# Kernel optimization log

Hardware: AMD Instinct MI355X
Metric: run time of the kernel (lower is better)

Reference implementation:

```python
import jax, jax.numpy as jnp
import numpy as np

MAT_MODE = [(0, 1), (0, 2), (1, 2)]   # plane axes per component (TensoRF VM)
VEC_MODE = [2, 1, 0]                  # line axis per component
DISTANCE_SCALE = 1.0
WHITE_BG = True


def _bilinear(plane, uv):
    """plane: [C,H,W]; uv: [P,2] in [-1,1] (uv[:,0]->W, uv[:,1]->H). align_corners=True."""
    H, W = plane.shape[-2], plane.shape[-1]
    x = (uv[:, 0] + 1.0) * 0.5 * (W - 1)
    y = (uv[:, 1] + 1.0) * 0.5 * (H - 1)
    x0 = jnp.clip(jnp.floor(x), 0, W - 2).astype(jnp.int32)
    y0 = jnp.clip(jnp.floor(y), 0, H - 2).astype(jnp.int32)
    wx = x - x0
    wy = y - y0
    v00 = plane[:, y0, x0]
    v01 = plane[:, y0, x0 + 1]
    v10 = plane[:, y0 + 1, x0]
    v11 = plane[:, y0 + 1, x0 + 1]
    top = v00 * (1 - wx) + v01 * wx
    bot = v10 * (1 - wx) + v11 * wx
    return top * (1 - wy) + bot * wy   # [C,P]


def _linear1d(line, t):
    """line: [C,L]; t: [P] in [-1,1]. align_corners=True."""
    L = line.shape[-1]
    x = (t + 1.0) * 0.5 * (L - 1)
    x0 = jnp.clip(jnp.floor(x), 0, L - 2).astype(jnp.int32)
    w = x - x0
    return line[:, x0] * (1 - w) + line[:, x0 + 1] * w   # [C,P]


def setup_inputs() -> dict:
    key = jax.random.key(0)
    ks = jax.random.split(key, 8)
    N_rays = 4096
    # camera origins on a sphere of radius 4, dirs aimed at points inside the box
    o = jax.random.normal(ks[0], (N_rays, 3), jnp.float32)
    o = o / jnp.linalg.norm(o, axis=-1, keepdims=True) * 4.0
    tgt = jax.random.uniform(ks[1], (N_rays, 3), jnp.float32, -0.5, 0.5)
    d = tgt - o
    d = d / jnp.linalg.norm(d, axis=-1, keepdims=True)
    rays = jnp.concatenate([o, d], axis=-1)
    return {
        "rays": rays,
        "density_plane": 0.1 * jax.random.normal(ks[2], (3, 16, 256, 256), jnp.float32),
        "density_line": 0.1 * jax.random.normal(ks[3], (3, 16, 256), jnp.float32),
        "app_plane": 0.1 * jax.random.normal(ks[4], (3, 24, 256, 256), jnp.float32),
        "app_line": 0.1 * jax.random.normal(ks[5], (3, 24, 256), jnp.float32),
        "basis_mat": 0.1 * jax.random.normal(ks[6], (72, 3), jnp.float32),
        "aabb": jnp.array([[-1.5, -1.5, -1.5], [1.5, 1.5, 1.5]], jnp.float32),
        "N_samples": 256,
    }


def reference(rays, density_plane, density_line, app_plane, app_line, basis_mat, aabb, N_samples):
    N = rays.shape[0]
    o, d = rays[:, :3], rays[:, 3:6]
    # ray / aabb intersection
    vec = jnp.where(jnp.abs(d) < 1e-6, 1e-6, d)
    rate_a = (aabb[1] - o) / vec
    rate_b = (aabb[0] - o) / vec
    t_min = jnp.clip(jnp.minimum(rate_a, rate_b).max(-1), 0.05)
    t_max = jnp.maximum(jnp.maximum(rate_a, rate_b).min(-1), t_min + 1e-3)
    s = jnp.linspace(0.0, 1.0, N_samples, dtype=jnp.float32)
    z = t_min[:, None] * (1.0 - s) + t_max[:, None] * s          # [N,S]
    dists = jnp.diff(z, axis=-1)
    dists = jnp.concatenate([dists, dists[:, -1:]], axis=-1)      # [N,S]
    pts = o[:, None, :] + d[:, None, :] * z[..., None]            # [N,S,3]
    coords = (pts - aabb[0]) / (aabb[1] - aabb[0]) * 2.0 - 1.0
    inside = jnp.all(jnp.abs(coords) <= 1.0, axis=-1)             # [N,S]
    cf = coords.reshape(-1, 3)                                    # [P,3]

    sigma_feat = 0.0
    app_feats = []
    for i in range(3):
        uv = cf[:, list(MAT_MODE[i])]
        w = cf[:, VEC_MODE[i]]
        sigma_feat = sigma_feat + (_bilinear(density_plane[i], uv) * _linear1d(density_line[i], w)).sum(0)
        app_feats.append(_bilinear(app_plane[i], uv) * _linear1d(app_line[i], w))
    app = jnp.concatenate(app_feats, axis=0).T                    # [P, 72]

    sigma = jax.nn.softplus(sigma_feat).reshape(N, -1) * inside   # [N,S]
    alpha = 1.0 - jnp.exp(-sigma * dists * DISTANCE_SCALE)        # [N,S]
    T = jnp.cumprod(1.0 - alpha + 1e-10, axis=-1)
    T = jnp.concatenate([jnp.ones_like(T[:, :1]), T[:, :-1]], axis=-1)
    weights = alpha * T                                           # [N,S]

    rgb = jax.nn.sigmoid(app @ basis_mat).reshape(N, -1, 3)       # [N,S,3]
    rgb_map = (weights[..., None] * rgb).sum(1)                   # [N,3]
    acc = weights.sum(-1)
    if WHITE_BG:
        rgb_map = rgb_map + (1.0 - acc)[..., None]
    rgb_map = jnp.clip(rgb_map, 0.0, 1.0)
    depth_map = (weights * z).sum(-1, keepdims=True)              # [N,1]
    return rgb_map, depth_map
```

## Files before the change

kernel.cpp:

```cpp
#include <hip/hip_runtime.h>
#include <hip/hip_fp16.h>
#include <cmath>

#define NRAYS 4096
#define NSAMP 256

static constexpr size_t DPT_B = 0;
static constexpr size_t DLT_B = 3145728;
static constexpr size_t APT_B = DLT_B + 24576;
static constexpr size_t ALT_B = APT_B + 6291456;
static constexpr size_t RAY_B = ALT_B + 24576;
static constexpr size_t WS_NEED = RAY_B + 131072;

typedef _Float16 __attribute__((ext_vector_type(2))) v2h;
typedef __attribute__((ext_vector_type(2))) float f32x2;

#if defined(__has_builtin)
#if __has_builtin(__builtin_amdgcn_cvt_scalef32_pk_f16_fp8)
#define HAS_SCVT 1
#endif
#endif
#ifndef HAS_SCVT
#define HAS_SCVT 0
#endif

__device__ __forceinline__ float dot2acc(__half2 a, __half2 b, float c) {
  return __builtin_amdgcn_fdot2(__builtin_bit_cast(v2h, a),
                                __builtin_bit_cast(v2h, b), c, false);
}

__device__ __forceinline__ __half2 lerp2(__half2 a, __half2 b, __half2 w) {
  return __hfma2(w, __hsub2(b, a), a);
}

__device__ __forceinline__ void ld8h(const __half* p, __half2 h[4]) {
  uint4 r = *(const uint4*)p;
  h[0] = __builtin_bit_cast(__half2, r.x);
  h[1] = __builtin_bit_cast(__half2, r.y);
  h[2] = __builtin_bit_cast(__half2, r.z);
  h[3] = __builtin_bit_cast(__half2, r.w);
}

__device__ __forceinline__ unsigned pack2h(float a, float b) {
  return __builtin_bit_cast(unsigned, __floats2half2_rn(a, b));
}

__device__ __forceinline__ void dec4f8h(unsigned w, __half2& h0, __half2& h1) {
#if HAS_SCVT
  v2h a = __builtin_amdgcn_cvt_scalef32_pk_f16_fp8((int)w, 1.0f, false);
  v2h b = __builtin_amdgcn_cvt_scalef32_pk_f16_fp8((int)w, 1.0f, true);
  h0 = __builtin_bit_cast(__half2, a);
  h1 = __builtin_bit_cast(__half2, b);
#else
  f32x2 lo = __builtin_amdgcn_cvt_pk_f32_fp8((int)w, false);
  f32x2 hi = __builtin_amdgcn_cvt_pk_f32_fp8((int)w, true);
  h0 = __floats2half2_rn(lo.x, lo.y);
  h1 = __floats2half2_rn(hi.x, hi.y);
#endif
}

__device__ __forceinline__ void dec8f8(uint2 q, __half2 h[4]) {
  dec4f8h(q.x, h[0], h[1]);
  dec4f8h(q.y, h[2], h[3]);
}

__device__ __forceinline__ void dec16f8(uint4 q, __half2 h[8]) {
  dec4f8h(q.x, h[0], h[1]);
  dec4f8h(q.y, h[2], h[3]);
  dec4f8h(q.z, h[4], h[5]);
  dec4f8h(q.w, h[6], h[7]);
}

__device__ __forceinline__ unsigned pk4f8(float a, float b, float c, float d) {
  int w = __builtin_amdgcn_cvt_pk_fp8_f32(a, b, 0, false);
  w = __builtin_amdgcn_cvt_pk_fp8_f32(c, d, w, true);
  return (unsigned)w;
}

__device__ __forceinline__ void grid_uv(float c, int& i0, float& w) {
  float f = (c + 1.0f) * 127.5f;
  float fl = floorf(f);
  fl = fminf(fmaxf(fl, 0.0f), 254.0f);
  i0 = (int)fl;
  w = f - fl;
}

__device__ __forceinline__ void bilin_w(float wx, float wy, __half2& W00,
                                        __half2& W01, __half2& W10, __half2& W11) {
  float ix = 1.0f - wx, iy = 1.0f - wy;
  W00 = __float2half2_rn(ix * iy);
  W01 = __float2half2_rn(wx * iy);
  W10 = __float2half2_rn(ix * wy);
  W11 = __float2half2_rn(wx * wy);
}

__global__ __launch_bounds__(256) void prep_kernel(
    const float* __restrict__ dp, const float* __restrict__ ap,
    const float* __restrict__ dl, const float* __restrict__ al,
    const float* __restrict__ rays, const float* __restrict__ aabb,
    unsigned char* __restrict__ dpt, unsigned char* __restrict__ apt,
    __half* __restrict__ dlt, unsigned char* __restrict__ alt,
    float4* __restrict__ rd) {
  int b = blockIdx.x, x = threadIdx.x;
  if (b < 768) {
    int i = b >> 8, y = b & 255;
    const float* src = dp + (size_t)(i * 16) * 65536 + y * 256 + x;
    float f[16];
#pragma unroll
    for (int c = 0; c < 16; ++c) f[c] = src[c * 65536];
    uint4 v;
    v.x = pk4f8(f[0], f[1], f[2], f[3]);
    v.y = pk4f8(f[4], f[5], f[6], f[7]);
    v.z = pk4f8(f[8], f[9], f[10], f[11]);
    v.w = pk4f8(f[12], f[13], f[14], f[15]);
    *(uint4*)(dpt + ((size_t)(i << 16) + (y << 8) + x) * 16) = v;
  } else if (b < 1536) {
    int t = b - 768;
    int i = t >> 8, y = t & 255;
    const float* src = ap + (size_t)(i * 24) * 65536 + y * 256 + x;
    float f[24];
#pragma unroll
    for (int c = 0; c < 24; ++c) f[c] = src[c * 65536];
    uint4 v0, v1;
    v0.x = pk4f8(f[0], f[1], f[2], f[3]);
    v0.y = pk4f8(f[4], f[5], f[6], f[7]);
    v0.z = pk4f8(f[8], f[9], f[10], f[11]);
    v0.w = pk4f8(f[12], f[13], f[14], f[15]);
    v1.x = pk4f8(f[16], f[17], f[18], f[19]);
    v1.y = pk4f8(f[20], f[21], f[22], f[23]);
    v1.z = 0u; v1.w = 0u;
    uint4* dst = (uint4*)(apt + ((size_t)(i << 16) + (y << 8) + x) * 32);
    dst[0] = v0; dst[1] = v1;
  } else if (b < 1539) {
    int i = b - 1536, l = x;
    float f[16];
#pragma unroll
    for (int c = 0; c < 16; ++c) f[c] = dl[(i * 16 + c) * 256 + l];
    uint4 v0, v1;
    v0.x = pack2h(f[0], f[1]);   v0.y = pack2h(f[2], f[3]);
    v0.z = pack2h(f[4], f[5]);   v0.w = pack2h(f[6], f[7]);
    v1.x = pack2h(f[8], f[9]);   v1.y = pack2h(f[10], f[11]);
    v1.z = pack2h(f[12], f[13]); v1.w = pack2h(f[14], f[15]);
    uint4* dst = (uint4*)(dlt + (i * 256 + l) * 16);
    dst[0] = v0; dst[1] = v1;
  } else if (b < 1542) {
    int i = b - 1539, l = x;
    float f[24];
#pragma unroll
    for (int c = 0; c < 24; ++c) f[c] = al[(i * 24 + c) * 256 + l];
    uint4 v0, v1;
    v0.x = pk4f8(f[0], f[1], f[2], f[3]);
    v0.y = pk4f8(f[4], f[5], f[6], f[7]);
    v0.z = pk4f8(f[8], f[9], f[10], f[11]);
    v0.w = pk4f8(f[12], f[13], f[14], f[15]);
    v1.x = pk4f8(f[16], f[17], f[18], f[19]);
    v1.y = pk4f8(f[20], f[21], f[22], f[23]);
    v1.z = 0u; v1.w = 0u;
    uint4* dst = (uint4*)(alt + (i * 256 + l) * 32);
    dst[0] = v0; dst[1] = v1;
  } else {
    int r = (b - 1542) * 256 + x;
    if (r < NRAYS) {
      float o0 = rays[r * 6 + 0], o1 = rays[r * 6 + 1], o2 = rays[r * 6 + 2];
      float d0 = rays[r * 6 + 3], d1 = rays[r * 6 + 4], d2 = rays[r * 6 + 5];
      float A0 = aabb[0], A1 = aabb[1], A2 = aabb[2];
      float B0 = aabb[3], B1 = aabb[4], B2 = aabb[5];
      float v0 = fabsf(d0) < 1e-6f ? 1e-6f : d0;
      float v1 = fabsf(d1) < 1e-6f ? 1e-6f : d1;
      float v2 = fabsf(d2) < 1e-6f ? 1e-6f : d2;
      float ra0 = (B0 - o0) / v0, rb0 = (A0 - o0) / v0;
      float ra1 = (B1 - o1) / v1, rb1 = (A1 - o1) / v1;
      float ra2 = (B2 - o2) / v2, rb2 = (A2 - o2) / v2;
      float tmin = fmaxf(fmaxf(fminf(ra0, rb0), fminf(ra1, rb1)), fminf(ra2, rb2));
      tmin = fmaxf(tmin, 0.05f);
      float tmax = fminf(fminf(fmaxf(ra0, rb0), fmaxf(ra1, rb1)), fmaxf(ra2, rb2));
      tmax = fmaxf(tmax, tmin + 0.001f);
      float dt = (tmax - tmin) * (1.0f / 255.0f);
      float s0 = 2.0f / (B0 - A0), s1 = 2.0f / (B1 - A1), s2 = 2.0f / (B2 - A2);
      float4 a2, b2;
      a2.x = (o0 - A0) * s0 - 1.0f; a2.y = (o1 - A1) * s1 - 1.0f;
      a2.z = (o2 - A2) * s2 - 1.0f; a2.w = tmin;
      b2.x = d0 * s0; b2.y = d1 * s1; b2.z = d2 * s2; b2.w = dt;
      rd[r * 2] = a2;
      rd[r * 2 + 1] = b2;
    }
  }
}

__device__ __forceinline__ float density_f8(const unsigned char* __restrict__ pl,
                                            const __half* __restrict__ ln,
                                            int x0, int y0, int l0,
                                            __half2 W00, __half2 W01,
                                            __half2 W10, __half2 W11,
                                            __half2 wl, int sub, float acc) {
  const unsigned char* p = pl + (size_t)((y0 * 256 + x0) << 4) + sub * 8;
  uint2 q00 = *(const uint2*)p;
  uint2 q01 = *(const uint2*)(p + 16);
  uint2 q10 = *(const uint2*)(p + 4096);
  uint2 q11 = *(const uint2*)(p + 4096 + 16);
  __half2 A[4], B[4], C[4], D[4], la[4], lb[4];
  dec8f8(q00, A); dec8f8(q01, B); dec8f8(q10, C); dec8f8(q11, D);
  const __half* lp = ln + (l0 << 4) + sub * 8;
  ld8h(lp, la); ld8h(lp + 16, lb);
#pragma unroll
  for (int r = 0; r < 4; ++r) {
    __half2 m = __hmul2(W00, A[r]);
    m = __hfma2(W01, B[r], m);
    m = __hfma2(W10, C[r], m);
    m = __hfma2(W11, D[r], m);
    __half2 l = lerp2(la[r], lb[r], wl);
    acc = dot2acc(m, l, acc);
  }
  return acc;
}

__device__ __forceinline__ void app_f8(const unsigned char* __restrict__ pl,
                                       const unsigned char* __restrict__ ln,
                                       const __half2* __restrict__ btR,
                                       const __half2* __restrict__ btG,
                                       const __half2* __restrict__ btB,
                                       int x0, int y0, int l0,
                                       __half2 W00, __half2 W01,
                                       __half2 W10, __half2 W11,
                                       __half2 wl, int sub,
                                       float& dr, float& dg, float& db) {
  const unsigned char* p = pl + ((size_t)(y0 * 256 + x0) << 5) + sub * 16;
  uint4 qA = *(const uint4*)p;
  uint4 qB = *(const uint4*)(p + 32);
  uint4 qC = *(const uint4*)(p + 8192);
  uint4 qD = *(const uint4*)(p + 8192 + 32);
  const unsigned char* lp = ln + (l0 << 5) + sub * 16;
  uint4 qLA = *(const uint4*)lp;
  uint4 qLB = *(const uint4*)(lp + 32);
  __half2 A[8], B[8], C[8], D[8], LA[8], LB[8];
  dec16f8(qA, A); dec16f8(qB, B); dec16f8(qC, C); dec16f8(qD, D);
  dec16f8(qLA, LA); dec16f8(qLB, LB);
#pragma unroll
  for (int r = 0; r < 8; ++r) {
    __half2 m = __hmul2(W00, A[r]);
    m = __hfma2(W01, B[r], m);
    m = __hfma2(W10, C[r], m);
    m = __hfma2(W11, D[r], m);
    __half2 l = lerp2(LA[r], LB[r], wl);
    __half2 av = __hmul2(m, l);
    dr = dot2acc(av, btR[r], dr);
    dg = dot2acc(av, btG[r], dg);
    db = dot2acc(av, btB[r], db);
  }
}

__global__ __launch_bounds__(512) void render_fused(
    const float4* __restrict__ rd, const float* __restrict__ basis,
    const unsigned char* __restrict__ dpt, const __half* __restrict__ dlt,
    const unsigned char* __restrict__ apt, const unsigned char* __restrict__ alt,
    float* __restrict__ out) {
  __shared__ __align__(16) __half bth[3][3][32];
  __shared__ __align__(16) float4 sm[NSAMP];
  int tid = threadIdx.x;
  if (tid < 288) {
    int k = tid / 96, rem = tid - k * 96;
    int m = rem >> 5, c = rem & 31;
    float v = (c < 24) ? basis[(m * 24 + c) * 3 + k] : 0.0f;
    bth[k][m][c] = __float2half(v);
  }

  int ray = blockIdx.x;
  int j = tid >> 1, sub = tid & 1;

  float4 ra = rd[ray * 2];
  float4 rb = rd[ray * 2 + 1];
  float z = fmaf((float)j, rb.w, ra.w);
  float c0 = fmaf(rb.x, z, ra.x);
  float c1 = fmaf(rb.y, z, ra.y);
  float c2 = fmaf(rb.z, z, ra.z);
  bool inside = (fabsf(c0) <= 1.0f) && (fabsf(c1) <= 1.0f) && (fabsf(c2) <= 1.0f);

  __syncthreads();

  float sig = 0.f, dr = 0.f, dg = 0.f, db = 0.f;
  if (inside) {
    int i0, i1, i2;
    float w0, w1, w2;
    grid_uv(c0, i0, w0);
    grid_uv(c1, i1, w1);
    grid_uv(c2, i2, w2);
    __half2 h0 = __float2half2_rn(w0);
    __half2 h1 = __float2half2_rn(w1);
    __half2 h2 = __float2half2_rn(w2);
    __half2 Wa00, Wa01, Wa10, Wa11;
    __half2 Wb00, Wb01, Wb10, Wb11;
    __half2 Wc00, Wc01, Wc10, Wc11;
    bilin_w(w0, w1, Wa00, Wa01, Wa10, Wa11);
    bilin_w(w0, w2, Wb00, Wb01, Wb10, Wb11);
    bilin_w(w1, w2, Wc00, Wc01, Wc10, Wc11);

    sig = density_f8(dpt + 0 * 1048576, dlt + 0 * 4096, i0, i1, i2,
                     Wa00, Wa01, Wa10, Wa11, h2, sub, sig);
    sig = density_f8(dpt + 1 * 1048576, dlt + 1 * 4096, i0, i2, i1,
                     Wb00, Wb01, Wb10, Wb11, h1, sub, sig);
    sig = density_f8(dpt + 2 * 1048576, dlt + 2 * 4096, i1, i2, i0,
                     Wc00, Wc01, Wc10, Wc11, h0, sub, sig);
    app_f8(apt + 0 * 2097152, alt + 0 * 8192,
           (const __half2*)&bth[0][0][sub * 16], (const __half2*)&bth[1][0][sub * 16],
           (const __half2*)&bth[2][0][sub * 16], i0, i1, i2,
           Wa00, Wa01, Wa10, Wa11, h2, sub, dr, dg, db);
    app_f8(apt + 1 * 2097152, alt + 1 * 8192,
           (const __half2*)&bth[0][1][sub * 16], (const __half2*)&bth[1][1][sub * 16],
           (const __half2*)&bth[2][1][sub * 16], i0, i2, i1,
           Wb00, Wb01, Wb10, Wb11, h1, sub, dr, dg, db);
    app_f8(apt + 2 * 2097152, alt + 2 * 8192,
           (const __half2*)&bth[0][2][sub * 16], (const __half2*)&bth[1][2][sub * 16],
           (const __half2*)&bth[2][2][sub * 16], i1, i2, i0,
           Wc00, Wc01, Wc10, Wc11, h0, sub, dr, dg, db);
  }
  sig += __shfl_xor(sig, 1, 64);
  dr += __shfl_xor(dr, 1, 64);
  dg += __shfl_xor(dg, 1, 64);
  db += __shfl_xor(db, 1, 64);

  if (sub == 0) {
    float e = __expf(-fabsf(sig));
    float sp = fmaxf(sig, 0.f) + __logf(1.0f + e);
    float4 sv;
    sv.x = inside ? (1.0f - __expf(-sp * rb.w)) : 0.0f;
    sv.y = __builtin_amdgcn_rcpf(1.0f + __expf(-dr));
    sv.z = __builtin_amdgcn_rcpf(1.0f + __expf(-dg));
    sv.w = __builtin_amdgcn_rcpf(1.0f + __expf(-db));
    sm[j] = sv;
  }
  __syncthreads();

  if (tid < 64) {
    int lane = tid;
    float tmin = ra.w, dt = rb.w;
    float C = 1.0f;
    float racc = 0.f, gacc = 0.f, bacc = 0.f, wsum = 0.f, dsum = 0.f;
    for (int q = 0; q < 4; ++q) {
      int jj = q * 64 + lane;
      float4 sv = sm[jj];
      float alpha = sv.x;
      float zz = fmaf((float)jj, dt, tmin);
      float p = 1.0f - alpha + 1e-10f;
#pragma unroll
      for (int off = 1; off < 64; off <<= 1) {
        float t = __shfl_up(p, off, 64);
        if (lane >= off) p *= t;
      }
      float tot = __shfl(p, 63, 64);
      float e = __shfl_up(p, 1, 64);
      if (lane == 0) e = 1.0f;
      float Tj = C * e;
      float w = alpha * Tj;
      racc += w * sv.y;
      gacc += w * sv.z;
      bacc += w * sv.w;
      wsum += w;
      dsum += w * zz;
      C *= tot;
    }
#pragma unroll
    for (int off = 32; off > 0; off >>= 1) {
      racc += __shfl_down(racc, off, 64);
      gacc += __shfl_down(gacc, off, 64);
      bacc += __shfl_down(bacc, off, 64);
      wsum += __shfl_down(wsum, off, 64);
      dsum += __shfl_down(dsum, off, 64);
    }
    if (lane == 0) {
      float bgw = 1.0f - wsum;
      out[ray * 3 + 0] = fminf(fmaxf(racc + bgw, 0.f), 1.f);
      out[ray * 3 + 1] = fminf(fmaxf(gacc + bgw, 0.f), 1.f);
      out[ray * 3 + 2] = fminf(fmaxf(bacc + bgw, 0.f), 1.f);
      out[NRAYS * 3 + ray] = dsum;
    }
  }
}

__device__ __forceinline__ float density_orig(const float* __restrict__ plane,
                                              const float* __restrict__ line,
                                              float cx, float cy, float cw) {
  int x0, y0, l0; float wx, wy, wl;
  grid_uv(cx, x0, wx); grid_uv(cy, y0, wy); grid_uv(cw, l0, wl);
  int base = y0 * 256 + x0;
  float s = 0.0f;
#pragma unroll 4
  for (int c = 0; c < 16; ++c) {
    const float* pc = plane + c * 65536;
    float v00 = pc[base], v01 = pc[base + 1];
    float v10 = pc[base + 256], v11 = pc[base + 257];
    float top = fmaf(wx, v01 - v00, v00);
    float bot = fmaf(wx, v11 - v10, v10);
    float mid = fmaf(wy, bot - top, top);
    float la = line[c * 256 + l0], lb = line[c * 256 + l0 + 1];
    float lv = fmaf(wl, lb - la, la);
    s += mid * lv;
  }
  return s;
}

__device__ __forceinline__ void app_orig(const float* __restrict__ plane,
                                         const float* __restrict__ line,
                                         const float* __restrict__ btR,
                                         const float* __restrict__ btG,
                                         const float* __restrict__ btB,
                                         float cx, float cy, float cw,
                                         float& dr, float& dg, float& db) {
  int x0, y0, l0; float wx, wy, wl;
  grid_uv(cx, x0, wx); grid_uv(cy, y0, wy); grid_uv(cw, l0, wl);
  int base = y0 * 256 + x0;
#pragma unroll 4
  for (int c = 0; c < 24; ++c) {
    const float* pc = plane + c * 65536;
    float v00 = pc[base], v01 = pc[base + 1];
    float v10 = pc[base + 256], v11 = pc[base + 257];
    float top = fmaf(wx, v01 - v00, v00);
    float bot = fmaf(wx, v11 - v10, v10);
    float mid = fmaf(wy, bot - top, top);
    float la = line[c * 256 + l0], lb = line[c * 256 + l0 + 1];
    float lv = fmaf(wl, lb - la, la);
    float av = mid * lv;
    dr += av * btR[c]; dg += av * btG[c]; db += av * btB[c];
  }
}

__global__ __launch_bounds__(256) void render_fallback(
    const float* __restrict__ rays, const float* __restrict__ basis,
    const float* __restrict__ aabb, const float* __restrict__ dplane,
    const float* __restrict__ dline, const float* __restrict__ aplane,
    const float* __restrict__ aline, float* __restrict__ out) {
  __shared__ float bt[3 * 72];
  int tid = threadIdx.x;
  if (tid < 216) {
    int k = tid / 72, r = tid - k * 72;
    bt[tid] = basis[r * 3 + k];
  }
  __syncthreads();
  int lane = tid & 63;
  int ray = blockIdx.x * 4 + (tid >> 6);

  float o0 = rays[ray * 6 + 0], o1 = rays[ray * 6 + 1], o2 = rays[ray * 6 + 2];
  float d0 = rays[ray * 6 + 3], d1 = rays[ray * 6 + 4], d2 = rays[ray * 6 + 5];
  float A0 = aabb[0], A1 = aabb[1], A2 = aabb[2];
  float B0 = aabb[3], B1 = aabb[4], B2 = aabb[5];
  float v0 = fabsf(d0) < 1e-6f ? 1e-6f : d0;
  float v1 = fabsf(d1) < 1e-6f ? 1e-6f : d1;
  float v2 = fabsf(d2) < 1e-6f ? 1e-6f : d2;
  float ra0 = (B0 - o0) / v0, rb0 = (A0 - o0) / v0;
  float ra1 = (B1 - o1) / v1, rb1 = (A1 - o1) / v1;
  float ra2 = (B2 - o2) / v2, rb2 = (A2 - o2) / v2;
  float tmin = fmaxf(fmaxf(fminf(ra0, rb0), fminf(ra1, rb1)), fminf(ra2, rb2));
  tmin = fmaxf(tmin, 0.05f);
  float tmax = fminf(fminf(fmaxf(ra0, rb0), fmaxf(ra1, rb1)), fmaxf(ra2, rb2));
  tmax = fmaxf(tmax, tmin + 0.001f);
  float dt = (tmax - tmin) * (1.0f / 255.0f);
  float s0 = 2.0f / (B0 - A0), s1 = 2.0f / (B1 - A1), s2 = 2.0f / (B2 - A2);

  float C = 1.0f;
  float racc = 0.f, gacc = 0.f, bacc = 0.f, wsum = 0.f, dsum = 0.f;
  for (int q = 0; q < 4; ++q) {
    int j = q * 64 + lane;
    float sfrac = (float)j * (1.0f / 255.0f);
    float z = tmin * (1.0f - sfrac) + tmax * sfrac;
    float c0 = (o0 + d0 * z - A0) * s0 - 1.0f;
    float c1 = (o1 + d1 * z - A1) * s1 - 1.0f;
    float c2 = (o2 + d2 * z - A2) * s2 - 1.0f;
    bool inside = (fabsf(c0) <= 1.0f) && (fabsf(c1) <= 1.0f) && (fabsf(c2) <= 1.0f);
    float alpha = 0.f, cr = 0.f, cg = 0.f, cb = 0.f;
    if (inside) {
      float sig = 0.f, dr = 0.f, dg = 0.f, db = 0.f;
      sig += density_orig(dplane + 0 * 1048576, dline + 0 * 4096, c0, c1, c2);
      sig += density_orig(dplane + 1 * 1048576, dline + 1 * 4096, c0, c2, c1);
      sig += density_orig(dplane + 2 * 1048576, dline + 2 * 4096, c1, c2, c0);
      app_orig(aplane + 0 * 1572864, aline + 0 * 6144,
               &bt[0 * 72 + 0], &bt[1 * 72 + 0], &bt[2 * 72 + 0],
               c0, c1, c2, dr, dg, db);
      app_orig(aplane + 1 * 1572864, aline + 1 * 6144,
               &bt[0 * 72 + 24], &bt[1 * 72 + 24], &bt[2 * 72 + 24],
               c0, c2, c1, dr, dg, db);
      app_orig(aplane + 2 * 1572864, aline + 2 * 6144,
               &bt[0 * 72 + 48], &bt[1 * 72 + 48], &bt[2 * 72 + 48],
               c1, c2, c0, dr, dg, db);
      float sp = fmaxf(sig, 0.f) + log1pf(expf(-fabsf(sig)));
      alpha = 1.0f - expf(-sp * dt);
      cr = 1.0f / (1.0f + expf(-dr));
      cg = 1.0f / (1.0f + expf(-dg));
      cb = 1.0f / (1.0f + expf(-db));
    }
    float p = 1.0f - alpha + 1e-10f;
#pragma unroll
    for (int off = 1; off < 64; off <<= 1) {
      float t = __shfl_up(p, off, 64);
      if (lane >= off) p *= t;
    }
    float tot = __shfl(p, 63, 64);
    float e = __shfl_up(p, 1, 64);
    if (lane == 0) e = 1.0f;
    float Tj = C * e;
    float w = alpha * Tj;
    racc += w * cr; gacc += w * cg; bacc += w * cb;
    wsum += w; dsum += w * z;
    C *= tot;
  }
#pragma unroll
  for (int off = 32; off > 0; off >>= 1) {
    racc += __shfl_down(racc, off, 64);
    gacc += __shfl_down(gacc, off, 64);
    bacc += __shfl_down(bacc, off, 64);
    wsum += __shfl_down(wsum, off, 64);
    dsum += __shfl_down(dsum, off, 64);
  }
  if (lane == 0) {
    float bgw = 1.0f - wsum;
    out[ray * 3 + 0] = fminf(fmaxf(racc + bgw, 0.f), 1.f);
    out[ray * 3 + 1] = fminf(fmaxf(gacc + bgw, 0.f), 1.f);
    out[ray * 3 + 2] = fminf(fmaxf(bacc + bgw, 0.f), 1.f);
    out[NRAYS * 3 + ray] = dsum;
  }
}

extern "C" void kernel_launch(void* const* d_in, const int* in_sizes, int n_in,
                              void* d_out, int out_size, void* d_ws, size_t ws_size,
                              hipStream_t stream) {
  const float* rays  = (const float*)d_in[0];
  const float* dp    = (const float*)d_in[1];
  const float* dl    = (const float*)d_in[2];
  const float* ap    = (const float*)d_in[3];
  const float* al    = (const float*)d_in[4];
  const float* basis = (const float*)d_in[5];
  const float* aabb  = (const float*)d_in[6];
  float* out = (float*)d_out;

  if (ws_size >= WS_NEED) {
    char* ws = (char*)d_ws;
    unsigned char* dpt = (unsigned char*)(ws + DPT_B);
    __half* dlt = (__half*)(ws + DLT_B);
    unsigned char* apt = (unsigned char*)(ws + APT_B);
    unsigned char* alt = (unsigned char*)(ws + ALT_B);
    float4* rayd = (float4*)(ws + RAY_B);
    prep_kernel<<<1558, 256, 0, stream>>>(dp, ap, dl, al, rays, aabb,
                                          dpt, apt, dlt, alt, rayd);
    render_fused<<<NRAYS, 512, 0, stream>>>(rayd, basis, dpt, dlt, apt, alt, out);
  } else {
    render_fallback<<<NRAYS / 4, 256, 0, stream>>>(
        rays, basis, aabb, dp, dl, ap, al, out);
  }
}
```

Measured before the change: 154.8 us.

## Split padded 32-byte FP8 appearance texels into 16+8 byte planes

Appearance plane and line features were stored as 32 bytes per texel in FP8, with 8 bytes of zero padding. They are now split into a 16-byte array for channels 0-15 and an 8-byte array for channels 16-23. Each of the two sub-lanes reads 8+4 bytes per corner instead of 16, and the basis table in shared memory is permuted to match the new channel order. This removes the padding from gather traffic and shrinks the appearance texture footprint, which may improve cache hit rates. The cost is twice as many separate, smaller load instructions per corner.

```diff
diff --git a/kernel.cpp b/kernel.cpp
--- a/kernel.cpp
+++ b/kernel.cpp
@@ -5,11 +5,13 @@
 #define NRAYS 4096
 #define NSAMP 256
 
-static constexpr size_t DPT_B = 0;
-static constexpr size_t DLT_B = 3145728;
-static constexpr size_t APT_B = DLT_B + 24576;
-static constexpr size_t ALT_B = APT_B + 6291456;
-static constexpr size_t RAY_B = ALT_B + 24576;
+static constexpr size_t DPT_B  = 0;
+static constexpr size_t DLT_B  = 3145728;
+static constexpr size_t APTA_B = DLT_B + 24576;
+static constexpr size_t APTB_B = APTA_B + 3145728;
+static constexpr size_t ALTA_B = APTB_B + 1572864;
+static constexpr size_t ALTB_B = ALTA_B + 12288;
+static constexpr size_t RAY_B  = ALTB_B + 6144;
 static constexpr size_t WS_NEED = RAY_B + 131072;
 
 typedef _Float16 __attribute__((ext_vector_type(2))) v2h;
@@ -64,13 +66,6 @@
   dec4f8h(q.y, h[2], h[3]);
 }
 
-__device__ __forceinline__ void dec16f8(uint4 q, __half2 h[8]) {
-  dec4f8h(q.x, h[0], h[1]);
-  dec4f8h(q.y, h[2], h[3]);
-  dec4f8h(q.z, h[4], h[5]);
-  dec4f8h(q.w, h[6], h[7]);
-}
-
 __device__ __forceinline__ unsigned pk4f8(float a, float b, float c, float d) {
   int w = __builtin_amdgcn_cvt_pk_fp8_f32(a, b, 0, false);
   w = __builtin_amdgcn_cvt_pk_fp8_f32(c, d, w, true);
@@ -98,8 +93,9 @@
     const float* __restrict__ dp, const float* __restrict__ ap,
     const float* __restrict__ dl, const float* __restrict__ al,
     const float* __restrict__ rays, const float* __restrict__ aabb,
-    unsigned char* __restrict__ dpt, unsigned char* __restrict__ apt,
-    __half* __restrict__ dlt, unsigned char* __restrict__ alt,
+    unsigned char* __restrict__ dpt, unsigned char* __restrict__ aptA,
+    unsigned char* __restrict__ aptB, __half* __restrict__ dlt,
+    unsigned char* __restrict__ altA, unsigned char* __restrict__ altB,
     float4* __restrict__ rd) {
   int b = blockIdx.x, x = threadIdx.x;
   if (b < 768) {
@@ -121,16 +117,17 @@
     float f[24];
 #pragma unroll
     for (int c = 0; c < 24; ++c) f[c] = src[c * 65536];
-    uint4 v0, v1;
-    v0.x = pk4f8(f[0], f[1], f[2], f[3]);
-    v0.y = pk4f8(f[4], f[5], f[6], f[7]);
-    v0.z = pk4f8(f[8], f[9], f[10], f[11]);
-    v0.w = pk4f8(f[12], f[13], f[14], f[15]);
-    v1.x = pk4f8(f[16], f[17], f[18], f[19]);
-    v1.y = pk4f8(f[20], f[21], f[22], f[23]);
-    v1.z = 0u; v1.w = 0u;
-    uint4* dst = (uint4*)(apt + ((size_t)(i << 16) + (y << 8) + x) * 32);
-    dst[0] = v0; dst[1] = v1;
+    uint4 vA;
+    vA.x = pk4f8(f[0], f[1], f[2], f[3]);
+    vA.y = pk4f8(f[4], f[5], f[6], f[7]);
+    vA.z = pk4f8(f[8], f[9], f[10], f[11]);
+    vA.w = pk4f8(f[12], f[13], f[14], f[15]);
+    uint2 vB;
+    vB.x = pk4f8(f[16], f[17], f[18], f[19]);
+    vB.y = pk4f8(f[20], f[21], f[22], f[23]);
+    size_t idx = (size_t)(i << 16) + (y << 8) + x;
+    *(uint4*)(aptA + idx * 16) = vA;
+    *(uint2*)(aptB + idx * 8) = vB;
   } else if (b < 1539) {
     int i = b - 1536, l = x;
     float f[16];
@@ -148,16 +145,16 @@
     float f[24];
 #pragma unroll
     for (int c = 0; c < 24; ++c) f[c] = al[(i * 24 + c) * 256 + l];
-    uint4 v0, v1;
-    v0.x = pk4f8(f[0], f[1], f[2], f[3]);
-    v0.y = pk4f8(f[4], f[5], f[6], f[7]);
-    v0.z = pk4f8(f[8], f[9], f[10], f[11]);
-    v0.w = pk4f8(f[12], f[13], f[14], f[15]);
-    v1.x = pk4f8(f[16], f[17], f[18], f[19]);
-    v1.y = pk4f8(f[20], f[21], f[22], f[23]);
-    v1.z = 0u; v1.w = 0u;
-    uint4* dst = (uint4*)(alt + (i * 256 + l) * 32);
-    dst[0] = v0; dst[1] = v1;
+    uint4 vA;
+    vA.x = pk4f8(f[0], f[1], f[2], f[3]);
+    vA.y = pk4f8(f[4], f[5], f[6], f[7]);
+    vA.z = pk4f8(f[8], f[9], f[10], f[11]);
+    vA.w = pk4f8(f[12], f[13], f[14], f[15]);
+    uint2 vB;
+    vB.x = pk4f8(f[16], f[17], f[18], f[19]);
+    vB.y = pk4f8(f[20], f[21], f[22], f[23]);
+    *(uint4*)(altA + (i * 256 + l) * 16) = vA;
+    *(uint2*)(altB + (i * 256 + l) * 8) = vB;
   } else {
     int r = (b - 1542) * 256 + x;
     if (r < NRAYS) {
@@ -214,29 +211,45 @@
   return acc;
 }
 
-__device__ __forceinline__ void app_f8(const unsigned char* __restrict__ pl,
-                                       const unsigned char* __restrict__ ln,
-                                       const __half2* __restrict__ btR,
-                                       const __half2* __restrict__ btG,
-                                       const __half2* __restrict__ btB,
-                                       int x0, int y0, int l0,
-                                       __half2 W00, __half2 W01,
-                                       __half2 W10, __half2 W11,
-                                       __half2 wl, int sub,
-                                       float& dr, float& dg, float& db) {
-  const unsigned char* p = pl + ((size_t)(y0 * 256 + x0) << 5) + sub * 16;
-  uint4 qA = *(const uint4*)p;
-  uint4 qB = *(const uint4*)(p + 32);
-  uint4 qC = *(const uint4*)(p + 8192);
-  uint4 qD = *(const uint4*)(p + 8192 + 32);
-  const unsigned char* lp = ln + (l0 << 5) + sub * 16;
-  uint4 qLA = *(const uint4*)lp;
-  uint4 qLB = *(const uint4*)(lp + 32);
-  __half2 A[8], B[8], C[8], D[8], LA[8], LB[8];
-  dec16f8(qA, A); dec16f8(qB, B); dec16f8(qC, C); dec16f8(qD, D);
-  dec16f8(qLA, LA); dec16f8(qLB, LB);
-#pragma unroll
-  for (int r = 0; r < 8; ++r) {
+__device__ __forceinline__ void app_f8s(const unsigned char* __restrict__ plA,
+                                        const unsigned char* __restrict__ plB,
+                                        const unsigned char* __restrict__ lnA,
+                                        const unsigned char* __restrict__ lnB,
+                                        const __half2* __restrict__ btR,
+                                        const __half2* __restrict__ btG,
+                                        const __half2* __restrict__ btB,
+                                        int x0, int y0, int l0,
+                                        __half2 W00, __half2 W01,
+                                        __half2 W10, __half2 W11,
+                                        __half2 wl, int sub,
+                                        float& dr, float& dg, float& db) {
+  size_t base = (size_t)(y0 * 256 + x0);
+  const unsigned char* pA = plA + (base << 4) + sub * 8;
+  uint2 a00 = *(const uint2*)pA;
+  uint2 a01 = *(const uint2*)(pA + 16);
+  uint2 a10 = *(const uint2*)(pA + 4096);
+  uint2 a11 = *(const uint2*)(pA + 4096 + 16);
+  const unsigned char* pB = plB + (base << 3) + sub * 4;
+  unsigned b00 = *(const unsigned*)pB;
+  unsigned b01 = *(const unsigned*)(pB + 8);
+  unsigned b10 = *(const unsigned*)(pB + 2048);
+  unsigned b11 = *(const unsigned*)(pB + 2048 + 8);
+  const unsigned char* lA = lnA + (l0 << 4) + sub * 8;
+  uint2 la2 = *(const uint2*)lA;
+  uint2 lb2 = *(const uint2*)(lA + 16);
+  const unsigned char* lB = lnB + (l0 << 3) + sub * 4;
+  unsigned la1 = *(const unsigned*)lB;
+  unsigned lb1 = *(const unsigned*)(lB + 8);
+
+  __half2 A[6], B[6], C[6], D[6], LA[6], LB[6];
+  dec8f8(a00, A); dec4f8h(b00, A[4], A[5]);
+  dec8f8(a01, B); dec4f8h(b01, B[4], B[5]);
+  dec8f8(a10, C); dec4f8h(b10, C[4], C[5]);
+  dec8f8(a11, D); dec4f8h(b11, D[4], D[5]);
+  dec8f8(la2, LA); dec4f8h(la1, LA[4], LA[5]);
+  dec8f8(lb2, LB); dec4f8h(lb1, LB[4], LB[5]);
+#pragma unroll
+  for (int r = 0; r < 6; ++r) {
     __half2 m = __hmul2(W00, A[r]);
     m = __hfma2(W01, B[r], m);
     m = __hfma2(W10, C[r], m);
@@ -252,16 +265,18 @@
 __global__ __launch_bounds__(512) void render_fused(
     const float4* __restrict__ rd, const float* __restrict__ basis,
     const unsigned char* __restrict__ dpt, const __half* __restrict__ dlt,
-    const unsigned char* __restrict__ apt, const unsigned char* __restrict__ alt,
+    const unsigned char* __restrict__ aptA, const unsigned char* __restrict__ aptB,
+    const unsigned char* __restrict__ altA, const unsigned char* __restrict__ altB,
     float* __restrict__ out) {
-  __shared__ __align__(16) __half bth[3][3][32];
+  __shared__ __align__(16) __half bthp[3][3][24];
   __shared__ __align__(16) float4 sm[NSAMP];
   int tid = threadIdx.x;
-  if (tid < 288) {
-    int k = tid / 96, rem = tid - k * 96;
-    int m = rem >> 5, c = rem & 31;
-    float v = (c < 24) ? basis[(m * 24 + c) * 3 + k] : 0.0f;
-    bth[k][m][c] = __float2half(v);
+  if (tid < 216) {
+    int k = tid / 72, rem = tid - k * 72;
+    int m = rem / 24, t = rem - m * 24;
+    int s = t / 12, u = t - s * 12;
+    int ch = (u < 8) ? (s * 8 + u) : (16 + s * 4 + (u - 8));
+    bthp[k][m][t] = __float2half(basis[(m * 24 + ch) * 3 + k]);
   }
 
   int ray = blockIdx.x;
@@ -300,18 +315,19 @@
                      Wb00, Wb01, Wb10, Wb11, h1, sub, sig);
     sig = density_f8(dpt + 2 * 1048576, dlt + 2 * 4096, i1, i2, i0,
                      Wc00, Wc01, Wc10, Wc11, h0, sub, sig);
-    app_f8(apt + 0 * 2097152, alt + 0 * 8192,
-           (const __half2*)&bth[0][0][sub * 16], (const __half2*)&bth[1][0][sub * 16],
-           (const __half2*)&bth[2][0][sub * 16], i0, i1, i2,
-           Wa00, Wa01, Wa10, Wa11, h2, sub, dr, dg, db);
-    app_f8(apt + 1 * 2097152, alt + 1 * 8192,
-           (const __half2*)&bth[0][1][sub * 16], (const __half2*)&bth[1][1][sub * 16],
-           (const __half2*)&bth[2][1][sub * 16], i0, i2, i1,
-           Wb00, Wb01, Wb10, Wb11, h1, sub, dr, dg, db);
-    app_f8(apt + 2 * 2097152, alt + 2 * 8192,
-           (const __half2*)&bth[0][2][sub * 16], (const __half2*)&bth[1][2][sub * 16],
-           (const __half2*)&bth[2][2][sub * 16], i1, i2, i0,
-           Wc00, Wc01, Wc10, Wc11, h0, sub, dr, dg, db);
+    int bo = sub * 12;
+    app_f8s(aptA + 0 * 1048576, aptB + 0 * 524288, altA + 0 * 4096, altB + 0 * 2048,
+            (const __half2*)&bthp[0][0][bo], (const __half2*)&bthp[1][0][bo],
+            (const __half2*)&bthp[2][0][bo], i0, i1, i2,
+            Wa00, Wa01, Wa10, Wa11, h2, sub, dr, dg, db);
+    app_f8s(aptA + 1 * 1048576, aptB + 1 * 524288, altA + 1 * 4096, altB + 1 * 2048,
+            (const __half2*)&bthp[0][1][bo], (const __half2*)&bthp[1][1][bo],
+            (const __half2*)&bthp[2][1][bo], i0, i2, i1,
+            Wb00, Wb01, Wb10, Wb11, h1, sub, dr, dg, db);
+    app_f8s(aptA + 2 * 1048576, aptB + 2 * 524288, altA + 2 * 4096, altB + 2 * 2048,
+            (const __half2*)&bthp[0][2][bo], (const __half2*)&bthp[1][2][bo],
+            (const __half2*)&bthp[2][2][bo], i1, i2, i0,
+            Wc00, Wc01, Wc10, Wc11, h0, sub, dr, dg, db);
   }
   sig += __shfl_xor(sig, 1, 64);
   dr += __shfl_xor(dr, 1, 64);
@@ -532,14 +548,17 @@
 
   if (ws_size >= WS_NEED) {
     char* ws = (char*)d_ws;
-    unsigned char* dpt = (unsigned char*)(ws + DPT_B);
-    __half* dlt = (__half*)(ws + DLT_B);
-    unsigned char* apt = (unsigned char*)(ws + APT_B);
-    unsigned char* alt = (unsigned char*)(ws + ALT_B);
-    float4* rayd = (float4*)(ws + RAY_B);
+    unsigned char* dpt  = (unsigned char*)(ws + DPT_B);
+    __half* dlt         = (__half*)(ws + DLT_B);
+    unsigned char* aptA = (unsigned char*)(ws + APTA_B);
+    unsigned char* aptB = (unsigned char*)(ws + APTB_B);
+    unsigned char* altA = (unsigned char*)(ws + ALTA_B);
+    unsigned char* altB = (unsigned char*)(ws + ALTB_B);
+    float4* rayd        = (float4*)(ws + RAY_B);
     prep_kernel<<<1558, 256, 0, stream>>>(dp, ap, dl, al, rays, aabb,
-                                          dpt, apt, dlt, alt, rayd);
-    render_fused<<<NRAYS, 512, 0, stream>>>(rayd, basis, dpt, dlt, apt, alt, out);
+                                          dpt, aptA, aptB, dlt, altA, altB, rayd);
+    render_fused<<<NRAYS, 512, 0, stream>>>(rayd, basis, dpt, dlt,
+                                            aptA, aptB, altA, altB, out);
   } else {
     render_fallback<<<NRAYS / 4, 256, 0, stream>>>(
         rays, basis, aabb, dp, dl, ap, al, out);
```

New measurement: 169.6 us. +9.6%, slower.

## Process one sample per thread instead of splitting channels across thread pairs

Applied to the files above, without the earlier changes.

Each thread now handles all channels of a sample, so blocks drop from 512 to 256 threads and the shuffle reduction between thread pairs goes away. Appearance channels are read as 24 packed bytes (uint4 plus uint2) with no padding to 32, and the basis table in shared memory shrinks to match. This halves thread count and skips the padded channels, but each thread now holds more registers and has more memory latency to hide per lane.

```diff
diff --git a/kernel.cpp b/kernel.cpp
--- a/kernel.cpp
+++ b/kernel.cpp
@@ -57,18 +57,6 @@
   h0 = __floats2half2_rn(lo.x, lo.y);
   h1 = __floats2half2_rn(hi.x, hi.y);
 #endif
-}
-
-__device__ __forceinline__ void dec8f8(uint2 q, __half2 h[4]) {
-  dec4f8h(q.x, h[0], h[1]);
-  dec4f8h(q.y, h[2], h[3]);
-}
-
-__device__ __forceinline__ void dec16f8(uint4 q, __half2 h[8]) {
-  dec4f8h(q.x, h[0], h[1]);
-  dec4f8h(q.y, h[2], h[3]);
-  dec4f8h(q.z, h[4], h[5]);
-  dec4f8h(q.w, h[6], h[7]);
 }
 
 __device__ __forceinline__ unsigned pk4f8(float a, float b, float c, float d) {
@@ -187,85 +175,115 @@
   }
 }
 
-__device__ __forceinline__ float density_f8(const unsigned char* __restrict__ pl,
-                                            const __half* __restrict__ ln,
-                                            int x0, int y0, int l0,
-                                            __half2 W00, __half2 W01,
-                                            __half2 W10, __half2 W11,
-                                            __half2 wl, int sub, float acc) {
-  const unsigned char* p = pl + (size_t)((y0 * 256 + x0) << 4) + sub * 8;
-  uint2 q00 = *(const uint2*)p;
-  uint2 q01 = *(const uint2*)(p + 16);
-  uint2 q10 = *(const uint2*)(p + 4096);
-  uint2 q11 = *(const uint2*)(p + 4096 + 16);
-  __half2 A[4], B[4], C[4], D[4], la[4], lb[4];
-  dec8f8(q00, A); dec8f8(q01, B); dec8f8(q10, C); dec8f8(q11, D);
-  const __half* lp = ln + (l0 << 4) + sub * 8;
-  ld8h(lp, la); ld8h(lp + 16, lb);
-#pragma unroll
-  for (int r = 0; r < 4; ++r) {
-    __half2 m = __hmul2(W00, A[r]);
-    m = __hfma2(W01, B[r], m);
-    m = __hfma2(W10, C[r], m);
-    m = __hfma2(W11, D[r], m);
-    __half2 l = lerp2(la[r], lb[r], wl);
-    acc = dot2acc(m, l, acc);
+__device__ __forceinline__ float density_full(const unsigned char* __restrict__ pl,
+                                              const __half* __restrict__ ln,
+                                              int x0, int y0, int l0,
+                                              __half2 W00, __half2 W01,
+                                              __half2 W10, __half2 W11,
+                                              __half2 wl, float acc) {
+  const unsigned char* p = pl + ((size_t)(y0 * 256 + x0) << 4);
+  uint4 q00 = *(const uint4*)p;
+  uint4 q01 = *(const uint4*)(p + 16);
+  uint4 q10 = *(const uint4*)(p + 4096);
+  uint4 q11 = *(const uint4*)(p + 4096 + 16);
+  const __half* lp = ln + (l0 << 4);
+  __half2 la[8], lb[8];
+  ld8h(lp, la); ld8h(lp + 8, la + 4);
+  ld8h(lp + 16, lb); ld8h(lp + 24, lb + 4);
+  unsigned c00[4] = {q00.x, q00.y, q00.z, q00.w};
+  unsigned c01[4] = {q01.x, q01.y, q01.z, q01.w};
+  unsigned c10[4] = {q10.x, q10.y, q10.z, q10.w};
+  unsigned c11[4] = {q11.x, q11.y, q11.z, q11.w};
+#pragma unroll
+  for (int g = 0; g < 4; ++g) {
+    __half2 a0, a1, b0, b1, c0, c1, d0, d1;
+    dec4f8h(c00[g], a0, a1);
+    dec4f8h(c01[g], b0, b1);
+    dec4f8h(c10[g], c0, c1);
+    dec4f8h(c11[g], d0, d1);
+    __half2 m0 = __hmul2(W00, a0);
+    m0 = __hfma2(W01, b0, m0);
+    m0 = __hfma2(W10, c0, m0);
+    m0 = __hfma2(W11, d0, m0);
+    __half2 m1 = __hmul2(W00, a1);
+    m1 = __hfma2(W01, b1, m1);
+    m1 = __hfma2(W10, c1, m1);
+    m1 = __hfma2(W11, d1, m1);
+    acc = dot2acc(m0, lerp2(la[2 * g], lb[2 * g], wl), acc);
+    acc = dot2acc(m1, lerp2(la[2 * g + 1], lb[2 * g + 1], wl), acc);
   }
   return acc;
 }
 
-__device__ __forceinline__ void app_f8(const unsigned char* __restrict__ pl,
-                                       const unsigned char* __restrict__ ln,
-                                       const __half2* __restrict__ btR,
-                                       const __half2* __restrict__ btG,
-                                       const __half2* __restrict__ btB,
-                                       int x0, int y0, int l0,
-                                       __half2 W00, __half2 W01,
-                                       __half2 W10, __half2 W11,
-                                       __half2 wl, int sub,
-                                       float& dr, float& dg, float& db) {
-  const unsigned char* p = pl + ((size_t)(y0 * 256 + x0) << 5) + sub * 16;
-  uint4 qA = *(const uint4*)p;
-  uint4 qB = *(const uint4*)(p + 32);
-  uint4 qC = *(const uint4*)(p + 8192);
-  uint4 qD = *(const uint4*)(p + 8192 + 32);
-  const unsigned char* lp = ln + (l0 << 5) + sub * 16;
-  uint4 qLA = *(const uint4*)lp;
-  uint4 qLB = *(const uint4*)(lp + 32);
-  __half2 A[8], B[8], C[8], D[8], LA[8], LB[8];
-  dec16f8(qA, A); dec16f8(qB, B); dec16f8(qC, C); dec16f8(qD, D);
-  dec16f8(qLA, LA); dec16f8(qLB, LB);
-#pragma unroll
-  for (int r = 0; r < 8; ++r) {
-    __half2 m = __hmul2(W00, A[r]);
-    m = __hfma2(W01, B[r], m);
-    m = __hfma2(W10, C[r], m);
-    m = __hfma2(W11, D[r], m);
-    __half2 l = lerp2(LA[r], LB[r], wl);
-    __half2 av = __hmul2(m, l);
-    dr = dot2acc(av, btR[r], dr);
-    dg = dot2acc(av, btG[r], dg);
-    db = dot2acc(av, btB[r], db);
-  }
-}
-
-__global__ __launch_bounds__(512) void render_fused(
+__device__ __forceinline__ void app_full(const unsigned char* __restrict__ pl,
+                                         const unsigned char* __restrict__ ln,
+                                         const __half2* __restrict__ btR,
+                                         const __half2* __restrict__ btG,
+                                         const __half2* __restrict__ btB,
+                                         int x0, int y0, int l0,
+                                         __half2 W00, __half2 W01,
+                                         __half2 W10, __half2 W11,
+                                         __half2 wl,
+                                         float& dr, float& dg, float& db) {
+  const unsigned char* p = pl + ((size_t)(y0 * 256 + x0) << 5);
+  uint4 h00 = *(const uint4*)p;         uint2 t00 = *(const uint2*)(p + 16);
+  uint4 h01 = *(const uint4*)(p + 32);  uint2 t01 = *(const uint2*)(p + 48);
+  uint4 h10 = *(const uint4*)(p + 8192);      uint2 t10 = *(const uint2*)(p + 8208);
+  uint4 h11 = *(const uint4*)(p + 8192 + 32); uint2 t11 = *(const uint2*)(p + 8192 + 48);
+  const unsigned char* lp = ln + (l0 << 5);
+  uint4 hl0 = *(const uint4*)lp;        uint2 tl0 = *(const uint2*)(lp + 16);
+  uint4 hl1 = *(const uint4*)(lp + 32); uint2 tl1 = *(const uint2*)(lp + 48);
+
+  unsigned c00[6] = {h00.x, h00.y, h00.z, h00.w, t00.x, t00.y};
+  unsigned c01[6] = {h01.x, h01.y, h01.z, h01.w, t01.x, t01.y};
+  unsigned c10[6] = {h10.x, h10.y, h10.z, h10.w, t10.x, t10.y};
+  unsigned c11[6] = {h11.x, h11.y, h11.z, h11.w, t11.x, t11.y};
+  unsigned l0w[6] = {hl0.x, hl0.y, hl0.z, hl0.w, tl0.x, tl0.y};
+  unsigned l1w[6] = {hl1.x, hl1.y, hl1.z, hl1.w, tl1.x, tl1.y};
+#pragma unroll
+  for (int g = 0; g < 6; ++g) {
+    __half2 a0, a1, b0, b1, c0, c1, d0, d1, p0, p1, q0, q1;
+    dec4f8h(c00[g], a0, a1);
+    dec4f8h(c01[g], b0, b1);
+    dec4f8h(c10[g], c0, c1);
+    dec4f8h(c11[g], d0, d1);
+    dec4f8h(l0w[g], p0, p1);
+    dec4f8h(l1w[g], q0, q1);
+    __half2 m0 = __hmul2(W00, a0);
+    m0 = __hfma2(W01, b0, m0);
+    m0 = __hfma2(W10, c0, m0);
+    m0 = __hfma2(W11, d0, m0);
+    __half2 m1 = __hmul2(W00, a1);
+    m1 = __hfma2(W01, b1, m1);
+    m1 = __hfma2(W10, c1, m1);
+    m1 = __hfma2(W11, d1, m1);
+    __half2 av0 = __hmul2(m0, lerp2(p0, q0, wl));
+    __half2 av1 = __hmul2(m1, lerp2(p1, q1, wl));
+    dr = dot2acc(av0, btR[2 * g], dr);
+    dg = dot2acc(av0, btG[2 * g], dg);
+    db = dot2acc(av0, btB[2 * g], db);
+    dr = dot2acc(av1, btR[2 * g + 1], dr);
+    dg = dot2acc(av1, btG[2 * g + 1], dg);
+    db = dot2acc(av1, btB[2 * g + 1], db);
+  }
+}
+
+__global__ __launch_bounds__(256) void render_fused(
     const float4* __restrict__ rd, const float* __restrict__ basis,
     const unsigned char* __restrict__ dpt, const __half* __restrict__ dlt,
     const unsigned char* __restrict__ apt, const unsigned char* __restrict__ alt,
     float* __restrict__ out) {
-  __shared__ __align__(16) __half bth[3][3][32];
+  __shared__ __align__(16) __half bth[3][3][24];
   __shared__ __align__(16) float4 sm[NSAMP];
   int tid = threadIdx.x;
-  if (tid < 288) {
-    int k = tid / 96, rem = tid - k * 96;
-    int m = rem >> 5, c = rem & 31;
-    float v = (c < 24) ? basis[(m * 24 + c) * 3 + k] : 0.0f;
-    bth[k][m][c] = __float2half(v);
+  if (tid < 216) {
+    int k = tid / 72, rem = tid - k * 72;
+    int m = rem / 24, c = rem - m * 24;
+    bth[k][m][c] = __float2half(basis[(m * 24 + c) * 3 + k]);
   }
 
   int ray = blockIdx.x;
-  int j = tid >> 1, sub = tid & 1;
+  int j = tid;
 
   float4 ra = rd[ray * 2];
   float4 rb = rd[ray * 2 + 1];
@@ -294,31 +312,27 @@
     bilin_w(w0, w2, Wb00, Wb01, Wb10, Wb11);
     bilin_w(w1, w2, Wc00, Wc01, Wc10, Wc11);
 
-    sig = density_f8(dpt + 0 * 1048576, dlt + 0 * 4096, i0, i1, i2,
-                     Wa00, Wa01, Wa10, Wa11, h2, sub, sig);
-    sig = density_f8(dpt + 1 * 1048576, dlt + 1 * 4096, i0, i2, i1,
-                     Wb00, Wb01, Wb10, Wb11, h1, sub, sig);
-    sig = density_f8(dpt + 2 * 1048576, dlt + 2 * 4096, i1, i2, i0,
-                     Wc00, Wc01, Wc10, Wc11, h0, sub, sig);
-    app_f8(apt + 0 * 2097152, alt + 0 * 8192,
-           (const __half2*)&bth[0][0][sub * 16], (const __half2*)&bth[1][0][sub * 16],
-           (const __half2*)&bth[2][0][sub * 16], i0, i1, i2,
-           Wa00, Wa01, Wa10, Wa11, h2, sub, dr, dg, db);
-    app_f8(apt + 1 * 2097152, alt + 1 * 8192,
-           (const __half2*)&bth[0][1][sub * 16], (const __half2*)&bth[1][1][sub * 16],
-           (const __half2*)&bth[2][1][sub * 16], i0, i2, i1,
-           Wb00, Wb01, Wb10, Wb11, h1, sub, dr, dg, db);
-    app_f8(apt + 2 * 2097152, alt + 2 * 8192,
-           (const __half2*)&bth[0][2][sub * 16], (const __half2*)&bth[1][2][sub * 16],
-           (const __half2*)&bth[2][2][sub * 16], i1, i2, i0,
-           Wc00, Wc01, Wc10, Wc11, h0, sub, dr, dg, db);
-  }
-  sig += __shfl_xor(sig, 1, 64);
-  dr += __shfl_xor(dr, 1, 64);
-  dg += __shfl_xor(dg, 1, 64);
-  db += __shfl_xor(db, 1, 64);
-
-  if (sub == 0) {
+    sig = density_full(dpt + 0 * 1048576, dlt + 0 * 4096, i0, i1, i2,
+                       Wa00, Wa01, Wa10, Wa11, h2, sig);
+    sig = density_full(dpt + 1 * 1048576, dlt + 1 * 4096, i0, i2, i1,
+                       Wb00, Wb01, Wb10, Wb11, h1, sig);
+    sig = density_full(dpt + 2 * 1048576, dlt + 2 * 4096, i1, i2, i0,
+                       Wc00, Wc01, Wc10, Wc11, h0, sig);
+    app_full(apt + 0 * 2097152, alt + 0 * 8192,
+             (const __half2*)&bth[0][0][0], (const __half2*)&bth[1][0][0],
+             (const __half2*)&bth[2][0][0], i0, i1, i2,
+             Wa00, Wa01, Wa10, Wa11, h2, dr, dg, db);
+    app_full(apt + 1 * 2097152, alt + 1 * 8192,
+             (const __half2*)&bth[0][1][0], (const __half2*)&bth[1][1][0],
+             (const __half2*)&bth[2][1][0], i0, i2, i1,
+             Wb00, Wb01, Wb10, Wb11, h1, dr, dg, db);
+    app_full(apt + 2 * 2097152, alt + 2 * 8192,
+             (const __half2*)&bth[0][2][0], (const __half2*)&bth[1][2][0],
+             (const __half2*)&bth[2][2][0], i1, i2, i0,
+             Wc00, Wc01, Wc10, Wc11, h0, dr, dg, db);
+  }
+
+  {
     float e = __expf(-fabsf(sig));
     float sp = fmaxf(sig, 0.f) + __logf(1.0f + e);
     float4 sv;
@@ -539,7 +553,7 @@
     float4* rayd = (float4*)(ws + RAY_B);
     prep_kernel<<<1558, 256, 0, stream>>>(dp, ap, dl, al, rays, aabb,
                                           dpt, apt, dlt, alt, rayd);
-    render_fused<<<NRAYS, 512, 0, stream>>>(rayd, basis, dpt, dlt, apt, alt, out);
+    render_fused<<<NRAYS, 256, 0, stream>>>(rayd, basis, dpt, dlt, apt, alt, out);
   } else {
     render_fallback<<<NRAYS / 4, 256, 0, stream>>>(
         rays, basis, aabb, dp, dl, ap, al, out);
```

Result: slower. 172.6 us (+11.5%).
